# Kernel optimization log

Measured on AMD Instinct MI355X. Metric: run time of the kernel, lower is better.

## Reference

```python
import jax, jax.numpy as jnp
import numpy as np

N, T, H, D = 32, 2048, 1024, 384

def setup_inputs() -> dict:
    key = jax.random.key(0)
    k1, k2, k3, k4, k5 = jax.random.split(key, 5)
    scale_h = 1.0 / np.sqrt(H)
    scale_d = 1.0 / np.sqrt(D)
    return {
        "gru_output": jax.random.normal(k1, (N, T, H), dtype=jnp.float32),
        "condition": jax.random.normal(k2, (N, D), dtype=jnp.float32),
        "W_h": jax.random.normal(k3, (H, H), dtype=jnp.float32) * scale_h,
        "W_c": jax.random.normal(k4, (D, H), dtype=jnp.float32) * scale_d,
        "bias": jnp.zeros((H,), dtype=jnp.float32),
        "v": jax.random.normal(k5, (H,), dtype=jnp.float32) * scale_h,
    }

def reference(gru_output, condition, W_h, W_c, bias, v):
    # h_proj: (N, T, H); c_proj: (N, 1, H)
    h_proj = jnp.einsum("nth,hk->ntk", gru_output, W_h)
    c_proj = jnp.einsum("nd,dk->nk", condition, W_c)[:, None, :]
    energy = jnp.tanh(h_proj + c_proj + bias)          # (N, T, H)
    scores = jnp.einsum("ntk,k->nt", energy, v)        # (N, T)
    weights = jax.nn.softmax(scores, axis=-1)          # (N, T)
    context = jnp.einsum("nth,nt->nh", gru_output, weights)  # (N, H)
    return context
```

## Files before the change

### kernel.cpp

```cpp
#include <hip/hip_runtime.h>
#include <hip/hip_bf16.h>

#define N_B 32
#define T_S 2048
#define H_D 1024
#define D_C 384
#define NT  (N_B * T_S)

typedef __attribute__((ext_vector_type(8))) short bf16x8;
typedef __attribute__((ext_vector_type(4))) float f32x4;

__device__ __forceinline__ ushort f2bf(float f) {
    union { float f; unsigned u; } x; x.f = f;
    unsigned u = x.u;
    unsigned r = (u + 0x7FFFu + ((u >> 16) & 1u)) >> 16;
    return (ushort)r;
}

__device__ __forceinline__ float fast_tanh(float x) {
    float e = __expf(2.0f * x);
    return 1.0f - 2.0f / (e + 1.0f);
}

__global__ __launch_bounds__(256) void transpose_kernel(
    const float* __restrict__ W, ushort* __restrict__ Wt)
{
    __shared__ ushort tile[64 * 66];
    const int bx = blockIdx.x & 15;
    const int by = blockIdx.x >> 4;
    const int t = threadIdx.x;
    #pragma unroll
    for (int i = 0; i < 16; ++i) {
        int idx = t + i * 256;
        int r = idx >> 6, c = idx & 63;
        tile[r * 66 + c] = f2bf(W[(size_t)(by * 64 + r) * H_D + bx * 64 + c]);
    }
    __syncthreads();
    #pragma unroll
    for (int i = 0; i < 16; ++i) {
        int idx = t + i * 256;
        int r = idx >> 6, c = idx & 63;
        Wt[(size_t)(bx * 64 + r) * H_D + by * 64 + c] = tile[c * 66 + r];
    }
}

__global__ __launch_bounds__(256) void cproj_kernel(
    const float* __restrict__ cond, const float* __restrict__ Wc,
    const float* __restrict__ bias, float* __restrict__ cproj)
{
    const int idx = blockIdx.x * 256 + threadIdx.x;
    const int n = idx >> 10, k = idx & 1023;
    float acc = bias[k];
    const float* cp = cond + n * D_C;
    for (int d = 0; d < D_C; ++d)
        acc = fmaf(cp[d], Wc[(size_t)d * H_D + k], acc);
    cproj[idx] = acc;
}

#define LDSS 40
__global__ __launch_bounds__(256) void gemm_score_kernel(
    const float* __restrict__ gru, const ushort* __restrict__ Wt,
    const float* __restrict__ cproj, const float* __restrict__ v,
    float* __restrict__ scores)
{
    __shared__ __align__(16) ushort As[128 * LDSS];
    __shared__ __align__(16) ushort Bt[128 * LDSS];
    const int kb = blockIdx.x;
    const int mb = blockIdx.y;
    const int m0 = mb * 128;
    const int nbatch = mb >> 4;
    const int t = threadIdx.x;
    const int lane = t & 63, wave = t >> 6;
    const int wm = wave & 1, wn = wave >> 1;
    const int q = lane >> 4, ln = lane & 15;

    f32x4 acc[4][4];
    #pragma unroll
    for (int i = 0; i < 4; ++i)
        #pragma unroll
        for (int j = 0; j < 4; ++j)
            acc[i][j] = (f32x4){0.f, 0.f, 0.f, 0.f};

    for (int h0 = 0; h0 < H_D; h0 += 32) {
        if (h0) __syncthreads();
        #pragma unroll
        for (int i = 0; i < 4; ++i) {
            int f = t + i * 256;
            int row = f >> 3, c4 = f & 7;
            const float4 val = *(const float4*)(gru + (size_t)(m0 + row) * H_D + h0 + c4 * 4);
            ushort4 o;
            o.x = f2bf(val.x); o.y = f2bf(val.y); o.z = f2bf(val.z); o.w = f2bf(val.w);
            *(ushort4*)(&As[row * LDSS + c4 * 4]) = o;
        }
        #pragma unroll
        for (int i = 0; i < 2; ++i) {
            int f = t + i * 256;
            int n = f >> 2, c = f & 3;
            uint4 wv = *(const uint4*)(Wt + (size_t)(kb * 128 + n) * H_D + h0 + c * 8);
            *(uint4*)(&Bt[n * LDSS + c * 8]) = wv;
        }
        __syncthreads();
        bf16x8 a[4], b[4];
        #pragma unroll
        for (int i = 0; i < 4; ++i)
            a[i] = *(const bf16x8*)(&As[(wm * 64 + i * 16 + ln) * LDSS + q * 8]);
        #pragma unroll
        for (int j = 0; j < 4; ++j)
            b[j] = *(const bf16x8*)(&Bt[(wn * 64 + j * 16 + ln) * LDSS + q * 8]);
        #pragma unroll
        for (int i = 0; i < 4; ++i)
            #pragma unroll
            for (int j = 0; j < 4; ++j)
                acc[i][j] = __builtin_amdgcn_mfma_f32_16x16x32_bf16(a[i], b[j], acc[i][j], 0, 0, 0);
    }

    float cpv[4], vv[4];
    const float* cpn = cproj + nbatch * H_D;
    #pragma unroll
    for (int j = 0; j < 4; ++j) {
        int col = kb * 128 + wn * 64 + j * 16 + ln;
        cpv[j] = cpn[col];
        vv[j] = v[col];
    }
    #pragma unroll
    for (int i = 0; i < 4; ++i) {
        float s0 = 0.f, s1 = 0.f, s2 = 0.f, s3 = 0.f;
        #pragma unroll
        for (int j = 0; j < 4; ++j) {
            s0 += fast_tanh(acc[i][j][0] + cpv[j]) * vv[j];
            s1 += fast_tanh(acc[i][j][1] + cpv[j]) * vv[j];
            s2 += fast_tanh(acc[i][j][2] + cpv[j]) * vv[j];
            s3 += fast_tanh(acc[i][j][3] + cpv[j]) * vv[j];
        }
        #pragma unroll
        for (int off = 1; off < 16; off <<= 1) {
            s0 += __shfl_xor(s0, off);
            s1 += __shfl_xor(s1, off);
            s2 += __shfl_xor(s2, off);
            s3 += __shfl_xor(s3, off);
        }
        if (ln == 0) {
            int mrow = m0 + wm * 64 + i * 16 + q * 4;
            atomicAdd(&scores[mrow + 0], s0);
            atomicAdd(&scores[mrow + 1], s1);
            atomicAdd(&scores[mrow + 2], s2);
            atomicAdd(&scores[mrow + 3], s3);
        }
    }
}

__global__ __launch_bounds__(256) void softmax_kernel(
    const float* __restrict__ scores, float* __restrict__ weights)
{
    const int n = blockIdx.x;
    const int t = threadIdx.x;
    __shared__ float red[256];
    float sv[8];
    float m = -1e30f;
    #pragma unroll
    for (int i = 0; i < 8; ++i) {
        sv[i] = scores[n * T_S + i * 256 + t];
        m = fmaxf(m, sv[i]);
    }
    red[t] = m; __syncthreads();
    for (int s = 128; s > 0; s >>= 1) {
        if (t < s) red[t] = fmaxf(red[t], red[t + s]);
        __syncthreads();
    }
    const float mx = red[0];
    __syncthreads();
    float sum = 0.f;
    #pragma unroll
    for (int i = 0; i < 8; ++i) { sv[i] = __expf(sv[i] - mx); sum += sv[i]; }
    red[t] = sum; __syncthreads();
    for (int s = 128; s > 0; s >>= 1) {
        if (t < s) red[t] += red[t + s];
        __syncthreads();
    }
    const float inv = 1.0f / red[0];
    #pragma unroll
    for (int i = 0; i < 8; ++i) weights[n * T_S + i * 256 + t] = sv[i] * inv;
}

__global__ __launch_bounds__(256) void context_kernel(
    const float* __restrict__ gru, const float* __restrict__ weights,
    float* __restrict__ out)
{
    const int tb = blockIdx.x;
    const int n  = blockIdx.y;
    const int t4 = threadIdx.x;
    float4 acc = make_float4(0.f, 0.f, 0.f, 0.f);
    const float* wp = weights + n * T_S + tb * 256;
    const float* gp = gru + (size_t)(n * T_S + tb * 256) * H_D + t4 * 4;
    for (int tt = 0; tt < 256; ++tt) {
        float w = wp[tt];
        float4 gv = *(const float4*)(gp + (size_t)tt * H_D);
        acc.x += w * gv.x; acc.y += w * gv.y;
        acc.z += w * gv.z; acc.w += w * gv.w;
    }
    float* op = out + n * H_D + t4 * 4;
    atomicAdd(op + 0, acc.x);
    atomicAdd(op + 1, acc.y);
    atomicAdd(op + 2, acc.z);
    atomicAdd(op + 3, acc.w);
}

extern "C" void kernel_launch(void* const* d_in, const int* in_sizes, int n_in,
                              void* d_out, int out_size, void* d_ws, size_t ws_size,
                              hipStream_t stream)
{
    const float* gru  = (const float*)d_in[0];
    const float* cond = (const float*)d_in[1];
    const float* W_h  = (const float*)d_in[2];
    const float* W_c  = (const float*)d_in[3];
    const float* bias = (const float*)d_in[4];
    const float* v    = (const float*)d_in[5];
    float* out = (float*)d_out;

    char* ws = (char*)d_ws;
    ushort* Wt     = (ushort*)ws;
    float*  cproj  = (float*)(ws + (2u << 20));
    float*  scores = (float*)(ws + (2u << 20) + (128u << 10));
    float*  wts    = (float*)(ws + (2u << 20) + (384u << 10));

    hipMemsetAsync(scores, 0, NT * sizeof(float), stream);
    hipMemsetAsync(out, 0, N_B * H_D * sizeof(float), stream);

    transpose_kernel<<<256, 256, 0, stream>>>(W_h, Wt);
    cproj_kernel<<<128, 256, 0, stream>>>(cond, W_c, bias, cproj);
    gemm_score_kernel<<<dim3(8, 512), 256, 0, stream>>>(gru, Wt, cproj, v, scores);
    softmax_kernel<<<N_B, 256, 0, stream>>>(scores, wts);
    context_kernel<<<dim3(8, N_B), 256, 0, stream>>>(gru, wts, out);
}
```

Before: 650.6 us.

## Pre-convert activations to bf16 and use direct global-to-LDS loads in GEMM

Adds a pass that converts the fp32 GRU output to bf16 once, so the score GEMM loads bf16 tiles straight into LDS with global_load_lds, using a 64-wide K step and an XOR-swizzled layout. Blocks are remapped so the eight N-tiles of one M-group run close together for L2 reuse. Score atomics become per-kb partial buffers that the softmax sums. The context kernel reads the bf16 copy with more blocks, and cproj uses split accumulators. This costs an extra full read and write pass over the activations plus a large workspace, and the context sum now runs on bf16 inputs, which loses precision.

```diff
diff --git a/kernel.cpp b/kernel.cpp
--- a/kernel.cpp
+++ b/kernel.cpp
@@ -9,6 +9,7 @@
 
 typedef __attribute__((ext_vector_type(8))) short bf16x8;
 typedef __attribute__((ext_vector_type(4))) float f32x4;
+typedef __attribute__((ext_vector_type(8))) unsigned short u16x8;
 
 __device__ __forceinline__ ushort f2bf(float f) {
     union { float f; unsigned u; } x; x.f = f;
@@ -17,9 +18,32 @@
     return (ushort)r;
 }
 
+__device__ __forceinline__ float bf2f(ushort u) {
+    union { unsigned u; float f; } x; x.u = ((unsigned)u) << 16;
+    return x.f;
+}
+
 __device__ __forceinline__ float fast_tanh(float x) {
     float e = __expf(2.0f * x);
     return 1.0f - 2.0f / (e + 1.0f);
+}
+
+__device__ __forceinline__ void gl2lds16(const void* g, void* l) {
+    __builtin_amdgcn_global_load_lds(
+        (const __attribute__((address_space(1))) void*)g,
+        (__attribute__((address_space(3))) void*)l, 16, 0, 0);
+}
+
+__global__ __launch_bounds__(256) void convert_kernel(
+    const float* __restrict__ g, ushort* __restrict__ gb)
+{
+    const size_t base = ((size_t)blockIdx.x * 256 + threadIdx.x) * 8;
+    float4 v0 = *(const float4*)(g + base);
+    float4 v1 = *(const float4*)(g + base + 4);
+    u16x8 o;
+    o[0] = f2bf(v0.x); o[1] = f2bf(v0.y); o[2] = f2bf(v0.z); o[3] = f2bf(v0.w);
+    o[4] = f2bf(v1.x); o[5] = f2bf(v1.y); o[6] = f2bf(v1.z); o[7] = f2bf(v1.w);
+    *(u16x8*)(gb + base) = o;
 }
 
 __global__ __launch_bounds__(256) void transpose_kernel(
@@ -50,29 +74,40 @@
 {
     const int idx = blockIdx.x * 256 + threadIdx.x;
     const int n = idx >> 10, k = idx & 1023;
-    float acc = bias[k];
+    float a0 = bias[k], a1 = 0.f, a2 = 0.f, a3 = 0.f;
     const float* cp = cond + n * D_C;
-    for (int d = 0; d < D_C; ++d)
-        acc = fmaf(cp[d], Wc[(size_t)d * H_D + k], acc);
-    cproj[idx] = acc;
-}
-
-#define LDSS 40
-__global__ __launch_bounds__(256) void gemm_score_kernel(
-    const float* __restrict__ gru, const ushort* __restrict__ Wt,
+    for (int d = 0; d < D_C; d += 4) {
+        a0 = fmaf(cp[d + 0], Wc[(size_t)(d + 0) * H_D + k], a0);
+        a1 = fmaf(cp[d + 1], Wc[(size_t)(d + 1) * H_D + k], a1);
+        a2 = fmaf(cp[d + 2], Wc[(size_t)(d + 2) * H_D + k], a2);
+        a3 = fmaf(cp[d + 3], Wc[(size_t)(d + 3) * H_D + k], a3);
+    }
+    cproj[idx] = (a0 + a1) + (a2 + a3);
+}
+
+__global__ __launch_bounds__(256) void gemm3_kernel(
+    const ushort* __restrict__ Ab, const ushort* __restrict__ Wt,
     const float* __restrict__ cproj, const float* __restrict__ v,
-    float* __restrict__ scores)
-{
-    __shared__ __align__(16) ushort As[128 * LDSS];
-    __shared__ __align__(16) ushort Bt[128 * LDSS];
-    const int kb = blockIdx.x;
-    const int mb = blockIdx.y;
+    float* __restrict__ spart)
+{
+    __shared__ __align__(16) ushort As[128 * 64];
+    __shared__ __align__(16) ushort Bs[128 * 64];
+    __shared__ float red[2][2][4][16];
+    const int id = blockIdx.x;
+    const int mb = (id & 7) + ((id >> 6) << 3);
+    const int kb = (id >> 3) & 7;
     const int m0 = mb * 128;
     const int nbatch = mb >> 4;
     const int t = threadIdx.x;
     const int lane = t & 63, wave = t >> 6;
     const int wm = wave & 1, wn = wave >> 1;
     const int q = lane >> 4, ln = lane & 15;
+    const int x7 = ln & 7;
+
+    const int srow = wave * 8 + (lane >> 3);
+    const int koff = ((lane & 7) ^ (lane >> 3)) * 8;
+    const ushort* ag = Ab + (size_t)(m0 + srow) * H_D + koff;
+    const ushort* bg = Wt + (size_t)(kb * 128 + srow) * H_D + koff;
 
     f32x4 acc[4][4];
     #pragma unroll
@@ -81,37 +116,33 @@
         for (int j = 0; j < 4; ++j)
             acc[i][j] = (f32x4){0.f, 0.f, 0.f, 0.f};
 
-    for (int h0 = 0; h0 < H_D; h0 += 32) {
+    for (int h0 = 0; h0 < H_D; h0 += 64) {
         if (h0) __syncthreads();
         #pragma unroll
         for (int i = 0; i < 4; ++i) {
-            int f = t + i * 256;
-            int row = f >> 3, c4 = f & 7;
-            const float4 val = *(const float4*)(gru + (size_t)(m0 + row) * H_D + h0 + c4 * 4);
-            ushort4 o;
-            o.x = f2bf(val.x); o.y = f2bf(val.y); o.z = f2bf(val.z); o.w = f2bf(val.w);
-            *(ushort4*)(&As[row * LDSS + c4 * 4]) = o;
-        }
-        #pragma unroll
-        for (int i = 0; i < 2; ++i) {
-            int f = t + i * 256;
-            int n = f >> 2, c = f & 3;
-            uint4 wv = *(const uint4*)(Wt + (size_t)(kb * 128 + n) * H_D + h0 + c * 8);
-            *(uint4*)(&Bt[n * LDSS + c * 8]) = wv;
+            gl2lds16(ag + h0 + i * 32 * H_D, As + i * 2048 + wave * 512);
+            gl2lds16(bg + h0 + i * 32 * H_D, Bs + i * 2048 + wave * 512);
         }
         __syncthreads();
-        bf16x8 a[4], b[4];
-        #pragma unroll
-        for (int i = 0; i < 4; ++i)
-            a[i] = *(const bf16x8*)(&As[(wm * 64 + i * 16 + ln) * LDSS + q * 8]);
-        #pragma unroll
-        for (int j = 0; j < 4; ++j)
-            b[j] = *(const bf16x8*)(&Bt[(wn * 64 + j * 16 + ln) * LDSS + q * 8]);
-        #pragma unroll
-        for (int i = 0; i < 4; ++i)
+        #pragma unroll
+        for (int kk = 0; kk < 2; ++kk) {
+            bf16x8 a[4], b[4];
             #pragma unroll
-            for (int j = 0; j < 4; ++j)
-                acc[i][j] = __builtin_amdgcn_mfma_f32_16x16x32_bf16(a[i], b[j], acc[i][j], 0, 0, 0);
+            for (int i = 0; i < 4; ++i) {
+                int row = wm * 64 + i * 16 + ln;
+                a[i] = *(const bf16x8*)(&As[row * 64 + (((kk << 2) + q) ^ x7) * 8]);
+            }
+            #pragma unroll
+            for (int j = 0; j < 4; ++j) {
+                int row = wn * 64 + j * 16 + ln;
+                b[j] = *(const bf16x8*)(&Bs[row * 64 + (((kk << 2) + q) ^ x7) * 8]);
+            }
+            #pragma unroll
+            for (int i = 0; i < 4; ++i)
+                #pragma unroll
+                for (int j = 0; j < 4; ++j)
+                    acc[i][j] = __builtin_amdgcn_mfma_f32_16x16x32_bf16(a[i], b[j], acc[i][j], 0, 0, 0);
+        }
     }
 
     float cpv[4], vv[4];
@@ -140,17 +171,23 @@
             s3 += __shfl_xor(s3, off);
         }
         if (ln == 0) {
-            int mrow = m0 + wm * 64 + i * 16 + q * 4;
-            atomicAdd(&scores[mrow + 0], s0);
-            atomicAdd(&scores[mrow + 1], s1);
-            atomicAdd(&scores[mrow + 2], s2);
-            atomicAdd(&scores[mrow + 3], s3);
-        }
-    }
-}
-
-__global__ __launch_bounds__(256) void softmax_kernel(
-    const float* __restrict__ scores, float* __restrict__ weights)
+            red[wm][wn][i][q * 4 + 0] = s0;
+            red[wm][wn][i][q * 4 + 1] = s1;
+            red[wm][wn][i][q * 4 + 2] = s2;
+            red[wm][wn][i][q * 4 + 3] = s3;
+        }
+    }
+    __syncthreads();
+    if (t < 128) {
+        int wm2 = t >> 6, idx = t & 63;
+        int i2 = idx >> 4, qr = idx & 15;
+        float val = red[wm2][0][i2][qr] + red[wm2][1][i2][qr];
+        spart[(size_t)kb * NT + m0 + wm2 * 64 + idx] = val;
+    }
+}
+
+__global__ __launch_bounds__(256) void softmax8_kernel(
+    const float* __restrict__ spart, float* __restrict__ weights)
 {
     const int n = blockIdx.x;
     const int t = threadIdx.x;
@@ -159,8 +196,12 @@
     float m = -1e30f;
     #pragma unroll
     for (int i = 0; i < 8; ++i) {
-        sv[i] = scores[n * T_S + i * 256 + t];
-        m = fmaxf(m, sv[i]);
+        int mrow = n * T_S + i * 256 + t;
+        float s = 0.f;
+        #pragma unroll
+        for (int kb = 0; kb < 8; ++kb) s += spart[(size_t)kb * NT + mrow];
+        sv[i] = s;
+        m = fmaxf(m, s);
     }
     red[t] = m; __syncthreads();
     for (int s = 128; s > 0; s >>= 1) {
@@ -182,27 +223,30 @@
     for (int i = 0; i < 8; ++i) weights[n * T_S + i * 256 + t] = sv[i] * inv;
 }
 
-__global__ __launch_bounds__(256) void context_kernel(
-    const float* __restrict__ gru, const float* __restrict__ weights,
+__global__ __launch_bounds__(256) void context2_kernel(
+    const ushort* __restrict__ Ab, const float* __restrict__ weights,
     float* __restrict__ out)
 {
     const int tb = blockIdx.x;
     const int n  = blockIdx.y;
-    const int t4 = threadIdx.x;
-    float4 acc = make_float4(0.f, 0.f, 0.f, 0.f);
-    const float* wp = weights + n * T_S + tb * 256;
-    const float* gp = gru + (size_t)(n * T_S + tb * 256) * H_D + t4 * 4;
-    for (int tt = 0; tt < 256; ++tt) {
+    const int t  = threadIdx.x;
+    float a0 = 0.f, a1 = 0.f, a2 = 0.f, a3 = 0.f;
+    const float* wp = weights + n * T_S + tb * 64;
+    const ushort* gp = Ab + (size_t)(n * T_S + tb * 64) * H_D + t * 4;
+    #pragma unroll 8
+    for (int tt = 0; tt < 64; ++tt) {
         float w = wp[tt];
-        float4 gv = *(const float4*)(gp + (size_t)tt * H_D);
-        acc.x += w * gv.x; acc.y += w * gv.y;
-        acc.z += w * gv.z; acc.w += w * gv.w;
-    }
-    float* op = out + n * H_D + t4 * 4;
-    atomicAdd(op + 0, acc.x);
-    atomicAdd(op + 1, acc.y);
-    atomicAdd(op + 2, acc.z);
-    atomicAdd(op + 3, acc.w);
+        ushort4 gv = *(const ushort4*)(gp + (size_t)tt * H_D);
+        a0 = fmaf(w, bf2f(gv.x), a0);
+        a1 = fmaf(w, bf2f(gv.y), a1);
+        a2 = fmaf(w, bf2f(gv.z), a2);
+        a3 = fmaf(w, bf2f(gv.w), a3);
+    }
+    float* op = out + n * H_D + t * 4;
+    atomicAdd(op + 0, a0);
+    atomicAdd(op + 1, a1);
+    atomicAdd(op + 2, a2);
+    atomicAdd(op + 3, a3);
 }
 
 extern "C" void kernel_launch(void* const* d_in, const int* in_sizes, int n_in,
@@ -218,17 +262,22 @@
     float* out = (float*)d_out;
 
     char* ws = (char*)d_ws;
-    ushort* Wt     = (ushort*)ws;
-    float*  cproj  = (float*)(ws + (2u << 20));
-    float*  scores = (float*)(ws + (2u << 20) + (128u << 10));
-    float*  wts    = (float*)(ws + (2u << 20) + (384u << 10));
-
-    hipMemsetAsync(scores, 0, NT * sizeof(float), stream);
+    const size_t szAb    = (size_t)NT * H_D * 2;
+    const size_t szWt    = (size_t)H_D * H_D * 2;
+    const size_t szCproj = (size_t)N_B * H_D * 4;
+    const size_t szSpart = (size_t)8 * NT * 4;
+
+    ushort* Ab    = (ushort*)ws;
+    ushort* Wt    = (ushort*)(ws + szAb);
+    float* cproj  = (float*)(ws + szAb + szWt);
+    float* spart  = (float*)(ws + szAb + szWt + szCproj);
+    float* wts    = (float*)(ws + szAb + szWt + szCproj + szSpart);
+
     hipMemsetAsync(out, 0, N_B * H_D * sizeof(float), stream);
-
+    convert_kernel<<<32768, 256, 0, stream>>>(gru, Ab);
     transpose_kernel<<<256, 256, 0, stream>>>(W_h, Wt);
     cproj_kernel<<<128, 256, 0, stream>>>(cond, W_c, bias, cproj);
-    gemm_score_kernel<<<dim3(8, 512), 256, 0, stream>>>(gru, Wt, cproj, v, scores);
-    softmax_kernel<<<N_B, 256, 0, stream>>>(scores, wts);
-    context_kernel<<<dim3(8, N_B), 256, 0, stream>>>(gru, wts, out);
-}
+    gemm3_kernel<<<4096, 256, 0, stream>>>(Ab, Wt, cproj, v, spart);
+    softmax8_kernel<<<N_B, 256, 0, stream>>>(spart, wts);
+    context2_kernel<<<dim3(32, N_B), 256, 0, stream>>>(Ab, wts, out);
+}
```

New measurement: 581.2 us. -10.7%, faster.
